# Kernel optimization log

Hardware: AMD Instinct MI355X
Metric: run time of the kernel (lower is better)

## Reference

```python
import jax, jax.numpy as jnp
import numpy as np
from jax import lax

B, L, D, H, N, V, K = 2, 1024, 512, 8, 4, 32000, 64
HD = D // H


def layer_norm(x, g, b, eps=1e-5):
    m = jnp.mean(x, axis=-1, keepdims=True)
    v = jnp.var(x, axis=-1, keepdims=True)
    return (x - m) * lax.rsqrt(v + eps) * g + b


def setup_inputs() -> dict:
    ks = jax.random.split(jax.random.key(0), 16)
    s = 0.02
    return {
        "x_q": jax.random.normal(ks[0], (B, L, D), jnp.float32),
        "x": jax.random.randint(ks[1], (B, L), 0, V, jnp.int32),
        "E_slots": jax.random.normal(ks[2], (V, D), jnp.float32),
        "rhos": jax.random.uniform(ks[3], (N,), jnp.float32, 0.9, 0.999),
        "C_seq": jax.random.uniform(ks[4], (B, L, N), jnp.float32),
        "c_base": jax.random.uniform(ks[5], (B, K, N), jnp.float32),
        "unique_slots": jax.random.randint(ks[6], (B, K), 0, V, jnp.int32),
        "pad_mask": jnp.ones((B, K), jnp.bool_),
        "Wq": jax.random.normal(ks[7], (D, D), jnp.float32) * s,
        "Wk": jax.random.normal(ks[8], (D, D), jnp.float32) * s,
        "Wv": jax.random.normal(ks[9], (D, D), jnp.float32) * s,
        "Wo": jax.random.normal(ks[10], (D, D), jnp.float32) * s,
        "W_pe": jax.random.normal(ks[11], (N, D), jnp.float32) * s,
        "ln_kv_g": jnp.ones((D,), jnp.float32),
        "ln_kv_b": jnp.zeros((D,), jnp.float32),
        "ln_q_g": jnp.ones((D,), jnp.float32),
        "ln_q_b": jnp.zeros((D,), jnp.float32),
    }


def reference(x_q, x, E_slots, rhos, C_seq, c_base, unique_slots, pad_mask,
              Wq, Wk, Wv, Wo, W_pe, ln_kv_g, ln_kv_b, ln_q_g, ln_q_b):
    # --- projections (dropout is eval-mode identity) ---
    memory_base = layer_norm(E_slots, ln_kv_g, ln_kv_b)          # [V,D]
    E_k = (memory_base @ Wk).reshape(V, H, HD)                   # [V,H,hd]
    E_v = (memory_base @ Wv).reshape(V, H, HD)
    P_gate = (C_seq + 1.0) @ W_pe                                # [B,L,D]
    Q = layer_norm(x_q * P_gate, ln_q_g, ln_q_b) @ Wq            # [B,L,D]

    # --- initial EMA state from history ---
    safe = jnp.maximum(unique_slots, 0)                          # [B,K]
    ek0 = E_k[safe]                                              # [B,K,H,hd]
    ev0 = E_v[safe]
    outer0 = ek0[..., :, None] * ev0[..., None, :]               # [B,K,H,hd,hd]
    cb = c_base * pad_mask[..., None].astype(c_base.dtype)
    S0 = jnp.einsum('bkn,bkhij->bhnij', cb, outer0).astype(jnp.float32)  # [B,H,N,hd,hd]

    W_pe_hn = W_pe.reshape(N, H, HD).transpose(1, 0, 2)          # [H,N,hd]
    rhos_b = rhos[None, None, :, None, None]

    Qh = Q.reshape(B, L, H, HD).transpose(1, 0, 2, 3)            # [L,B,H,hd]
    toks = x.T                                                   # [L,B]

    def step(S, inp):
        q_t, tok = inp                                           # [B,H,hd], [B]
        S = S * rhos_b                                           # decay
        q_mod = q_t[:, :, None, :] * W_pe_hn[None]               # [B,H,N,hd]
        o_t = jnp.einsum('bhnd,bhnde->bhe', q_mod, S)            # sum over n, contract d
        ek_t = E_k[tok]                                          # [B,H,hd]
        ev_t = E_v[tok]
        outer = ek_t[..., :, None] * ev_t[..., None, :]          # [B,H,hd,hd]
        S = S + outer[:, :, None]                                # broadcast over N
        return S, o_t

    _, O = lax.scan(step, S0, (Qh, toks))                        # O: [L,B,H,hd]
    O = O.transpose(1, 0, 2, 3).reshape(B, L, D)
    return O @ Wo
```

## Files before the change

kernel.cpp:

```cpp
#include <hip/hip_runtime.h>
#include <stdint.h>

namespace {

constexpr int B = 2, L = 1024, D = 512, H = 8, N = 4, KSL = 64;
constexpr int CHK = 64;
constexpr int NCK = L / CHK;
constexpr int ROWS = B * L + B * KSL;

static_assert(D == 512 && N == 4, "layout assumptions");

typedef _Float16 half8 __attribute__((ext_vector_type(8)));
typedef _Float16 half4v __attribute__((ext_vector_type(4)));
typedef _Float16 half2t __attribute__((ext_vector_type(2)));
typedef float f32x4 __attribute__((ext_vector_type(4)));

__device__ __forceinline__ void gld16(_Float16* lds_dst, const _Float16* gsrc) {
  __builtin_amdgcn_global_load_lds(
      (const __attribute__((address_space(1))) unsigned int*)gsrc,
      (__attribute__((address_space(3))) unsigned int*)lds_dst, 16, 0, 0);
}

__global__ __launch_bounds__(256) void k_pre(
    const float* __restrict__ Wk, const float* __restrict__ Wv,
    const float* __restrict__ Wq, const float* __restrict__ Wo,
    _Float16* __restrict__ WTh,
    const float* __restrict__ E_slots, const int* __restrict__ x,
    const int* __restrict__ uniq, const float* __restrict__ kv_g,
    const float* __restrict__ kv_b, _Float16* __restrict__ lnEh,
    const float* __restrict__ x_q, const float* __restrict__ C_seq,
    const float* __restrict__ W_pe, const float* __restrict__ q_g,
    const float* __restrict__ q_b, _Float16* __restrict__ lnqh) {
  __shared__ _Float16 trh[64 * 66];
  __shared__ float red[8];
  int bid = blockIdx.x;
  int t = threadIdx.x;

  if (bid < 256) {
    int widx = bid >> 6, tile = bid & 63;
    int k0 = (tile >> 3) * 64, n0 = (tile & 7) * 64;
    const float* W = widx == 0 ? Wk : widx == 1 ? Wv : widx == 2 ? Wq : Wo;
#pragma unroll
    for (int i = 0; i < 16; ++i) {
      int idx = t + i * 256, r = idx >> 6, c = idx & 63;
      trh[c * 66 + r] = (_Float16)W[(size_t)(k0 + r) * 512 + n0 + c];
    }
    __syncthreads();
    _Float16* WT = WTh + (size_t)widx * 512 * 512;
#pragma unroll
    for (int i = 0; i < 8; ++i) {
      int idx = t + i * 256, rr = idx >> 5, cc = (idx & 31) * 2;
      half2t v = {trh[rr * 66 + cc], trh[rr * 66 + cc + 1]};
      *(half2t*)&WT[(size_t)(n0 + rr) * 512 + k0 + cc] = v;
    }
    return;
  }

  float vx, vy;
  const float* g;
  const float* bb;
  _Float16* dst;
  int d0 = t * 2;
  if (bid < 256 + ROWS) {
    int r = bid - 256;
    int idx;
    if (r < B * L) {
      idx = x[r];
    } else {
      int u = uniq[r - B * L];
      idx = u > 0 ? u : 0;
    }
    float2 v = *(const float2*)(E_slots + (size_t)idx * D + d0);
    vx = v.x;
    vy = v.y;
    g = kv_g; bb = kv_b;
    dst = lnEh + (size_t)r * D + d0;
  } else {
    int r = bid - 256 - ROWS;
    float c0 = C_seq[r * 4 + 0] + 1.f;
    float c1 = C_seq[r * 4 + 1] + 1.f;
    float c2 = C_seq[r * 4 + 2] + 1.f;
    float c3 = C_seq[r * 4 + 3] + 1.f;
    float p0 = c0 * W_pe[d0] + c1 * W_pe[512 + d0] + c2 * W_pe[1024 + d0] + c3 * W_pe[1536 + d0];
    float p1 = c0 * W_pe[d0 + 1] + c1 * W_pe[513 + d0] + c2 * W_pe[1025 + d0] + c3 * W_pe[1537 + d0];
    float2 xv = *(const float2*)(x_q + (size_t)r * D + d0);
    vx = xv.x * p0;
    vy = xv.y * p1;
    g = q_g; bb = q_b;
    dst = lnqh + (size_t)r * D + d0;
  }
  float s = vx + vy;
  float s2 = vx * vx + vy * vy;
#pragma unroll
  for (int o = 32; o > 0; o >>= 1) {
    s += __shfl_down(s, o);
    s2 += __shfl_down(s2, o);
  }
  if ((t & 63) == 0) {
    red[(t >> 6) * 2] = s;
    red[(t >> 6) * 2 + 1] = s2;
  }
  __syncthreads();
  float S = red[0] + red[2] + red[4] + red[6];
  float S2 = red[1] + red[3] + red[5] + red[7];
  float m = S * (1.f / D);
  float inv = rsqrtf(S2 * (1.f / D) - m * m + 1e-5f);
  half2t o2;
  o2.x = (_Float16)((vx - m) * inv * g[d0] + bb[d0]);
  o2.y = (_Float16)((vy - m) * inv * g[d0 + 1] + bb[d0 + 1]);
  *(half2t*)dst = o2;
}

__global__ __launch_bounds__(256) void k_gemm3(
    const _Float16* __restrict__ A0, const _Float16* __restrict__ Wt0, _Float16* __restrict__ C0, int M0,
    const _Float16* __restrict__ A1, const _Float16* __restrict__ Wt1, _Float16* __restrict__ C1, int M1,
    const _Float16* __restrict__ A2, const _Float16* __restrict__ Wt2, _Float16* __restrict__ C2, int M2) {
  const _Float16* A;
  const _Float16* Wt;
  _Float16* C;
  int M;
  int z = blockIdx.z;
  if (z == 0) { A = A0; Wt = Wt0; C = C0; M = M0; }
  else if (z == 1) { A = A1; Wt = Wt1; C = C1; M = M1; }
  else { A = A2; Wt = Wt2; C = C2; M = M2; }
  int m0 = blockIdx.y * 64;
  if (m0 >= M) return;
  int n0 = blockIdx.x * 64;

  __shared__ _Float16 As[2][64 * 64];
  __shared__ _Float16 Ws[2][64 * 64];
  int t = threadIdx.x;
  int lane = t & 63, w = t >> 6;
  int wr = (w >> 1) * 32, wc = (w & 1) * 32;
  int fr = lane & 15, kg = (lane >> 4) * 8;
  int kq = kg >> 3, fx = fr & 7;
  int pA = kq ^ fx, pB = (4 + kq) ^ fx;

  int srow = t >> 3;
  int sseg = ((t & 7) ^ (srow & 7)) * 8;
  int wbase = w * 512;

  const _Float16* gA = A + (size_t)(m0 + srow) * 512 + sseg;
  const _Float16* gB = Wt + (size_t)(n0 + srow) * 512 + sseg;

  f32x4 zero4 = {0.f, 0.f, 0.f, 0.f};
  f32x4 acc[2][2];
#pragma unroll
  for (int i = 0; i < 2; ++i)
#pragma unroll
    for (int j = 0; j < 2; ++j) acc[i][j] = zero4;

  gld16(&As[0][wbase], gA);
  gld16(&As[0][wbase + 2048], gA + 32 * 512);
  gld16(&Ws[0][wbase], gB);
  gld16(&Ws[0][wbase + 2048], gB + 32 * 512);
  __syncthreads();

  int buf = 0;
  for (int s8 = 0; s8 < 8; ++s8) {
    if (s8 < 7) {
      int k0 = (s8 + 1) * 64;
      gld16(&As[buf ^ 1][wbase], gA + k0);
      gld16(&As[buf ^ 1][wbase + 2048], gA + 32 * 512 + k0);
      gld16(&Ws[buf ^ 1][wbase], gB + k0);
      gld16(&Ws[buf ^ 1][wbase + 2048], gB + 32 * 512 + k0);
    }
    half8 af[2][2], bf[2][2];
#pragma unroll
    for (int mt = 0; mt < 2; ++mt) {
      int row = wr + mt * 16 + fr;
      af[mt][0] = *(const half8*)&As[buf][row * 64 + pA * 8];
      af[mt][1] = *(const half8*)&As[buf][row * 64 + pB * 8];
    }
#pragma unroll
    for (int nt = 0; nt < 2; ++nt) {
      int row = wc + nt * 16 + fr;
      bf[nt][0] = *(const half8*)&Ws[buf][row * 64 + pA * 8];
      bf[nt][1] = *(const half8*)&Ws[buf][row * 64 + pB * 8];
    }
#pragma unroll
    for (int mt = 0; mt < 2; ++mt)
#pragma unroll
      for (int nt = 0; nt < 2; ++nt) {
        acc[mt][nt] = __builtin_amdgcn_mfma_f32_16x16x32_f16(af[mt][0], bf[nt][0], acc[mt][nt], 0, 0, 0);
        acc[mt][nt] = __builtin_amdgcn_mfma_f32_16x16x32_f16(af[mt][1], bf[nt][1], acc[mt][nt], 0, 0, 0);
      }
    if (s8 < 7) __syncthreads();
    buf ^= 1;
  }
  int crow = (lane >> 4) * 4, ccol = lane & 15;
#pragma unroll
  for (int mt = 0; mt < 2; ++mt)
#pragma unroll
    for (int nt = 0; nt < 2; ++nt)
#pragma unroll
      for (int r = 0; r < 4; ++r)
        C[(size_t)(m0 + wr + mt * 16 + crow + r) * 512 + n0 + wc + nt * 16 + ccol] =
            (_Float16)acc[mt][nt][r];
}

__global__ __launch_bounds__(256) void k_gemm64(const _Float16* __restrict__ A,
                                                const _Float16* __restrict__ Wt,
                                                float* __restrict__ C) {
  int m0 = blockIdx.y * 64, n0 = blockIdx.x * 64;
  __shared__ _Float16 As[2][64 * 64];
  __shared__ _Float16 Ws[2][64 * 64];
  int t = threadIdx.x;
  int lane = t & 63, w = t >> 6;
  int wr = (w >> 1) * 32, wc = (w & 1) * 32;
  int fr = lane & 15, kg = (lane >> 4) * 8;
  int kq = kg >> 3, fx = fr & 7;
  int pA = kq ^ fx, pB = (4 + kq) ^ fx;

  int srow = t >> 3;
  int sseg = ((t & 7) ^ (srow & 7)) * 8;
  int wbase = w * 512;

  const _Float16* gA = A + (size_t)(m0 + srow) * 512 + sseg;
  const _Float16* gB = Wt + (size_t)(n0 + srow) * 512 + sseg;

  f32x4 zero4 = {0.f, 0.f, 0.f, 0.f};
  f32x4 acc[2][2];
#pragma unroll
  for (int i = 0; i < 2; ++i)
#pragma unroll
    for (int j = 0; j < 2; ++j) acc[i][j] = zero4;

  gld16(&As[0][wbase], gA);
  gld16(&As[0][wbase + 2048], gA + 32 * 512);
  gld16(&Ws[0][wbase], gB);
  gld16(&Ws[0][wbase + 2048], gB + 32 * 512);
  __syncthreads();

  int buf = 0;
  for (int s8 = 0; s8 < 8; ++s8) {
    if (s8 < 7) {
      int k0 = (s8 + 1) * 64;
      gld16(&As[buf ^ 1][wbase], gA + k0);
      gld16(&As[buf ^ 1][wbase + 2048], gA + 32 * 512 + k0);
      gld16(&Ws[buf ^ 1][wbase], gB + k0);
      gld16(&Ws[buf ^ 1][wbase + 2048], gB + 32 * 512 + k0);
    }
    half8 af[2][2], bf[2][2];
#pragma unroll
    for (int mt = 0; mt < 2; ++mt) {
      int row = wr + mt * 16 + fr;
      af[mt][0] = *(const half8*)&As[buf][row * 64 + pA * 8];
      af[mt][1] = *(const half8*)&As[buf][row * 64 + pB * 8];
    }
#pragma unroll
    for (int nt = 0; nt < 2; ++nt) {
      int row = wc + nt * 16 + fr;
      bf[nt][0] = *(const half8*)&Ws[buf][row * 64 + pA * 8];
      bf[nt][1] = *(const half8*)&Ws[buf][row * 64 + pB * 8];
    }
#pragma unroll
    for (int mt = 0; mt < 2; ++mt)
#pragma unroll
      for (int nt = 0; nt < 2; ++nt) {
        acc[mt][nt] = __builtin_amdgcn_mfma_f32_16x16x32_f16(af[mt][0], bf[nt][0], acc[mt][nt], 0, 0, 0);
        acc[mt][nt] = __builtin_amdgcn_mfma_f32_16x16x32_f16(af[mt][1], bf[nt][1], acc[mt][nt], 0, 0, 0);
      }
    if (s8 < 7) __syncthreads();
    buf ^= 1;
  }
  int crow = (lane >> 4) * 4, ccol = lane & 15;
#pragma unroll
  for (int mt = 0; mt < 2; ++mt)
#pragma unroll
    for (int nt = 0; nt < 2; ++nt)
#pragma unroll
      for (int r = 0; r < 4; ++r)
        C[(size_t)(m0 + wr + mt * 16 + crow + r) * 512 + n0 + wc + nt * 16 + ccol] =
            acc[mt][nt][r];
}

__global__ __launch_bounds__(256) void k_dct(const _Float16* __restrict__ EKh,
                                             const _Float16* __restrict__ EVh,
                                             const float* __restrict__ rhos,
                                             const float* __restrict__ c_base,
                                             _Float16* __restrict__ DCt,
                                             _Float16* __restrict__ S0t) {
  constexpr int LDH = 72;
  __shared__ _Float16 ekt[64 * LDH];
  __shared__ _Float16 evt[64 * LDH];
  __shared__ _Float16 dtab[4][64];
  int bid = blockIdx.x;
  int t = threadIdx.x;
  bool is_s0 = bid >= B * H * NCK;
  int row = t >> 2, seg = (t & 3) * 16;
  size_t grow;
  if (!is_s0) {
    int c = bid % NCK, h = (bid / NCK) % H, b = bid / (NCK * H);
    grow = (size_t)(b * L + c * CHK + row) * 512 + h * 64 + seg;
    int nn = t >> 6, uu = t & 63;
    dtab[nn][uu] = (_Float16)exp2f((float)(CHK - uu) * log2f(rhos[nn]));
  } else {
    int bh = bid - B * H * NCK;
    int h = bh % H, b = bh / H;
    grow = (size_t)(B * L + b * KSL + row) * 512 + h * 64 + seg;
    int nn = t >> 6, uu = t & 63;
    dtab[nn][uu] = (_Float16)c_base[(b * KSL + uu) * N + nn];
  }
  half8 e0 = *(const half8*)(EKh + grow);
  half8 e1 = *(const half8*)(EKh + grow + 8);
  half8 v0 = *(const half8*)(EVh + grow);
  half8 v1 = *(const half8*)(EVh + grow + 8);
#pragma unroll
  for (int i = 0; i < 8; ++i) {
    ekt[(seg + i) * LDH + row] = e0[i];
    ekt[(seg + 8 + i) * LDH + row] = e1[i];
    evt[(seg + i) * LDH + row] = v0[i];
    evt[(seg + 8 + i) * LDH + row] = v1[i];
  }
  __syncthreads();

  int lane = t & 63, w = t >> 6;
  int wr = (w >> 1) * 32, wc = (w & 1) * 32;
  int fr = lane & 15, kg = (lane >> 4) * 8;
  int crow = (lane >> 4) * 4, ccol = lane & 15;

  half8 ef[2][2], bf[2][2];
#pragma unroll
  for (int mt = 0; mt < 2; ++mt)
#pragma unroll
    for (int ks = 0; ks < 2; ++ks)
      ef[mt][ks] = *(const half8*)&evt[(wr + mt * 16 + fr) * LDH + ks * 32 + kg];
#pragma unroll
  for (int nt = 0; nt < 2; ++nt)
#pragma unroll
    for (int ks = 0; ks < 2; ++ks)
      bf[nt][ks] = *(const half8*)&ekt[(wc + nt * 16 + fr) * LDH + ks * 32 + kg];

  f32x4 zero4 = {0.f, 0.f, 0.f, 0.f};
#pragma unroll
  for (int n = 0; n < 4; ++n) {
    half8 dec0 = *(const half8*)&dtab[n][kg];
    half8 dec1 = *(const half8*)&dtab[n][32 + kg];
    half8 af0a = ef[0][0] * dec0, af0b = ef[0][1] * dec1;
    half8 af1a = ef[1][0] * dec0, af1b = ef[1][1] * dec1;
    f32x4 acc[2][2];
#pragma unroll
    for (int i = 0; i < 2; ++i)
#pragma unroll
      for (int j = 0; j < 2; ++j) acc[i][j] = zero4;
#pragma unroll
    for (int nt = 0; nt < 2; ++nt) {
      acc[0][nt] = __builtin_amdgcn_mfma_f32_16x16x32_f16(af0a, bf[nt][0], acc[0][nt], 0, 0, 0);
      acc[0][nt] = __builtin_amdgcn_mfma_f32_16x16x32_f16(af0b, bf[nt][1], acc[0][nt], 0, 0, 0);
      acc[1][nt] = __builtin_amdgcn_mfma_f32_16x16x32_f16(af1a, bf[nt][0], acc[1][nt], 0, 0, 0);
      acc[1][nt] = __builtin_amdgcn_mfma_f32_16x16x32_f16(af1b, bf[nt][1], acc[1][nt], 0, 0, 0);
    }
    _Float16* dp = is_s0 ? S0t + ((size_t)(bid - B * H * NCK) * N + n) * 4096
                         : DCt + ((size_t)bid * N + n) * 4096;
#pragma unroll
    for (int mt = 0; mt < 2; ++mt)
#pragma unroll
      for (int nt = 0; nt < 2; ++nt)
#pragma unroll
        for (int r = 0; r < 4; ++r)
          dp[(wr + mt * 16 + crow + r) * 64 + wc + nt * 16 + ccol] = (_Float16)acc[mt][nt][r];
  }
}

__global__ void k_gscan(const _Float16* __restrict__ S0t, const _Float16* __restrict__ DCt,
                        const float* __restrict__ rhos, _Float16* __restrict__ GT) {
  int bhn = blockIdx.x >> 2, sl = blockIdx.x & 3;
  int n = bhn % N, bh = bhn / N;
  float rho = rhos[n];
  float rhoC = exp2f(64.f * log2f(rho));
  int off = sl * 1024 + threadIdx.x * 4;
  half4v dc[NCK];
#pragma unroll
  for (int c = 0; c < NCK; ++c)
    dc[c] = *(const half4v*)(DCt + ((size_t)(bh * NCK + c) * N + n) * 4096 + off);
  half4v s0 = *(const half4v*)(S0t + (size_t)bhn * 4096 + off);
  float gv[4];
#pragma unroll
  for (int i = 0; i < 4; ++i) gv[i] = rho * (float)s0[i];
  _Float16* gp = GT + (size_t)bhn * NCK * 4096 + off;
#pragma unroll
  for (int cc = 0; cc < NCK; ++cc) {
    half4v o;
#pragma unroll
    for (int i = 0; i < 4; ++i) o[i] = (_Float16)gv[i];
    *(half4v*)(gp + (size_t)cc * 4096) = o;
#pragma unroll
    for (int i = 0; i < 4; ++i) gv[i] = rhoC * gv[i] + (float)dc[cc][i];
  }
}

__global__ __launch_bounds__(256) void k_chunk(
    const _Float16* __restrict__ Qh, const _Float16* __restrict__ EKh,
    const _Float16* __restrict__ EVh, const _Float16* __restrict__ GT,
    const float* __restrict__ W_pe, const float* __restrict__ rhos,
    _Float16* __restrict__ OAh) {
  int bid = blockIdx.x;
  int c = bid % NCK, h = (bid / NCK) % H, b = bid / (NCK * H);
  constexpr int LDH = 72;
  __shared__ _Float16 qs[64 * LDH];
  __shared__ _Float16 eks[64 * LDH];
  __shared__ _Float16 evt[64 * LDH];
  __shared__ _Float16 gts[4][64 * LDH];
  __shared__ _Float16 wsm[64 * LDH];
  __shared__ _Float16 wpeh[4][64];
  __shared__ float rup[4][64];
  __shared__ float rvi[4][64];
  int t = threadIdx.x;
  {
    int row = t >> 2, seg = (t & 3) * 16;
    size_t grow = (size_t)(b * L + c * CHK + row) * 512 + h * 64 + seg;
    half8 q0 = *(const half8*)(Qh + grow);
    half8 q1 = *(const half8*)(Qh + grow + 8);
    half8 k0 = *(const half8*)(EKh + grow);
    half8 k1 = *(const half8*)(EKh + grow + 8);
    half8 v0 = *(const half8*)(EVh + grow);
    half8 v1 = *(const half8*)(EVh + grow + 8);
    *(half8*)&qs[row * LDH + seg] = q0;
    *(half8*)&qs[row * LDH + seg + 8] = q1;
    *(half8*)&eks[row * LDH + seg] = k0;
    *(half8*)&eks[row * LDH + seg + 8] = k1;
#pragma unroll
    for (int i = 0; i < 8; ++i) {
      evt[(seg + i) * LDH + row] = v0[i];
      evt[(seg + 8 + i) * LDH + row] = v1[i];
    }
#pragma unroll
    for (int n = 0; n < 4; ++n) {
      const _Float16* gpp = GT + (((size_t)(b * H + h) * N + n) * NCK + c) * 4096 + row * 64 + seg;
      *(half8*)&gts[n][row * LDH + seg] = *(const half8*)gpp;
      *(half8*)&gts[n][row * LDH + seg + 8] = *(const half8*)(gpp + 8);
    }
    int nn = t >> 6, dd = t & 63;
    float l2r = log2f(rhos[nn]);
    wpeh[nn][dd] = (_Float16)W_pe[nn * 512 + h * 64 + dd];
    rup[nn][dd] = exp2f((float)dd * l2r);
    rvi[nn][dd] = exp2f(-(float)dd * l2r);
  }
  __syncthreads();

  int lane = t & 63, w = t >> 6;
  int u0 = w * 16;
  int fr = lane & 15, kg = (lane >> 4) * 8;
  int crow = (lane >> 4) * 4, ccol = lane & 15;

  half8 qf0 = *(const half8*)&qs[(u0 + fr) * LDH + kg];
  half8 qf1 = *(const half8*)&qs[(u0 + fr) * LDH + 32 + kg];

  f32x4 zero4 = {0.f, 0.f, 0.f, 0.f};
  f32x4 oa[4], wacc[4];
#pragma unroll
  for (int i = 0; i < 4; ++i) { oa[i] = zero4; wacc[i] = zero4; }

#pragma unroll
  for (int n = 0; n < 4; ++n) {
    half8 am0 = qf0 * (*(const half8*)&wpeh[n][kg]);
    half8 am1 = qf1 * (*(const half8*)&wpeh[n][32 + kg]);
    float ru[4];
#pragma unroll
    for (int r = 0; r < 4; ++r) ru[r] = rup[n][u0 + crow + r];
#pragma unroll
    for (int et = 0; et < 4; ++et) {
      f32x4 ta = zero4;
      ta = __builtin_amdgcn_mfma_f32_16x16x32_f16(
          am0, *(const half8*)&gts[n][(et * 16 + fr) * LDH + kg], ta, 0, 0, 0);
      ta = __builtin_amdgcn_mfma_f32_16x16x32_f16(
          am1, *(const half8*)&gts[n][(et * 16 + fr) * LDH + 32 + kg], ta, 0, 0, 0);
#pragma unroll
      for (int r = 0; r < 4; ++r) oa[et][r] += ru[r] * ta[r];
    }
#pragma unroll
    for (int vt = 0; vt < 4; ++vt) {
      f32x4 sa = zero4;
      sa = __builtin_amdgcn_mfma_f32_16x16x32_f16(
          am0, *(const half8*)&eks[(vt * 16 + fr) * LDH + kg], sa, 0, 0, 0);
      sa = __builtin_amdgcn_mfma_f32_16x16x32_f16(
          am1, *(const half8*)&eks[(vt * 16 + fr) * LDH + 32 + kg], sa, 0, 0, 0);
      int v = vt * 16 + ccol;
      float rv = rvi[n][v];
#pragma unroll
      for (int r = 0; r < 4; ++r) {
        int u = u0 + crow + r;
        float coef = (v < u) ? ru[r] * rv : 0.f;
        wacc[vt][r] += coef * sa[r];
      }
    }
  }
#pragma unroll
  for (int vt = 0; vt < 4; ++vt)
#pragma unroll
    for (int r = 0; r < 4; ++r)
      wsm[(u0 + crow + r) * LDH + vt * 16 + ccol] = (_Float16)wacc[vt][r];
  half8 wf0 = *(const half8*)&wsm[(u0 + fr) * LDH + kg];
  half8 wf1 = *(const half8*)&wsm[(u0 + fr) * LDH + 32 + kg];
#pragma unroll
  for (int et = 0; et < 4; ++et) {
    oa[et] = __builtin_amdgcn_mfma_f32_16x16x32_f16(
        wf0, *(const half8*)&evt[(et * 16 + fr) * LDH + kg], oa[et], 0, 0, 0);
    oa[et] = __builtin_amdgcn_mfma_f32_16x16x32_f16(
        wf1, *(const half8*)&evt[(et * 16 + fr) * LDH + 32 + kg], oa[et], 0, 0, 0);
  }
#pragma unroll
  for (int et = 0; et < 4; ++et)
#pragma unroll
    for (int r = 0; r < 4; ++r)
      OAh[(size_t)(b * L + c * CHK + u0 + crow + r) * 512 + h * 64 + et * 16 + ccol] =
          (_Float16)oa[et][r];
}

}

extern "C" void kernel_launch(void* const* d_in, const int* in_sizes, int n_in,
                              void* d_out, int out_size, void* d_ws, size_t ws_size,
                              hipStream_t stream) {
  const float* x_q = (const float*)d_in[0];
  const int* x = (const int*)d_in[1];
  const float* E_slots = (const float*)d_in[2];
  const float* rhos = (const float*)d_in[3];
  const float* C_seq = (const float*)d_in[4];
  const float* c_base = (const float*)d_in[5];
  const int* uniq = (const int*)d_in[6];
  const float* Wq = (const float*)d_in[8];
  const float* Wk = (const float*)d_in[9];
  const float* Wv = (const float*)d_in[10];
  const float* Wo = (const float*)d_in[11];
  const float* W_pe = (const float*)d_in[12];
  const float* ln_kv_g = (const float*)d_in[13];
  const float* ln_kv_b = (const float*)d_in[14];
  const float* ln_q_g = (const float*)d_in[15];
  const float* ln_q_b = (const float*)d_in[16];
  float* out = (float*)d_out;

  _Float16* hb = (_Float16*)d_ws;
  _Float16* lnEh = hb;
  _Float16* lnqh = lnEh + 1114112;
  _Float16* WTh = lnqh + 1048576;
  _Float16* EKh = WTh + 1048576;
  _Float16* EVh = EKh + 1114112;
  _Float16* Qh = EVh + 1114112;
  _Float16* DCt = Qh + 1048576;
  _Float16* S0t = DCt + 4194304;
  _Float16* GT = S0t + 262144;
  _Float16* OAh = GT + 4194304;

  const _Float16* WTk = WTh;
  const _Float16* WTv = WTh + 262144;
  const _Float16* WTq = WTh + 524288;
  const _Float16* WTo = WTh + 786432;

  k_pre<<<256 + ROWS + B * L, 256, 0, stream>>>(
      Wk, Wv, Wq, Wo, WTh, E_slots, x, uniq, ln_kv_g, ln_kv_b, lnEh,
      x_q, C_seq, W_pe, ln_q_g, ln_q_b, lnqh);
  k_gemm3<<<dim3(8, 34, 3), 256, 0, stream>>>(lnEh, WTk, EKh, ROWS,
                                              lnEh, WTv, EVh, ROWS,
                                              lnqh, WTq, Qh, B * L);
  k_dct<<<B * H * NCK + B * H, 256, 0, stream>>>(EKh, EVh, rhos, c_base, DCt, S0t);
  k_gscan<<<B * H * N * 4, 256, 0, stream>>>(S0t, DCt, rhos, GT);
  k_chunk<<<B * H * NCK, 256, 0, stream>>>(Qh, EKh, EVh, GT, W_pe, rhos, OAh);
  k_gemm64<<<dim3(8, 32), 256, 0, stream>>>(OAh, WTo, out);
}
```

Measured before the change: 44.63 us.

## Fuse K/V projection GEMMs with chunk outer-product kernel

Merges the separate K and V projection blocks into one block that shares the A tile and computes both accumulators. The per-chunk decayed outer-product (DCt/S0t) work is then done in the same block from registers through shared memory, which removes the k_dct launch and its reload of EKh/EVh. In exchange each block uses more registers and shared memory, which may reduce occupancy, and the fused blocks carry a longer serial tail.

```diff
diff --git a/kernel.cpp b/kernel.cpp
--- a/kernel.cpp
+++ b/kernel.cpp
@@ -111,92 +111,230 @@
   *(half2t*)dst = o2;
 }
 
-__global__ __launch_bounds__(256) void k_gemm3(
-    const _Float16* __restrict__ A0, const _Float16* __restrict__ Wt0, _Float16* __restrict__ C0, int M0,
-    const _Float16* __restrict__ A1, const _Float16* __restrict__ Wt1, _Float16* __restrict__ C1, int M1,
-    const _Float16* __restrict__ A2, const _Float16* __restrict__ Wt2, _Float16* __restrict__ C2, int M2) {
-  const _Float16* A;
-  const _Float16* Wt;
-  _Float16* C;
-  int M;
+__global__ __launch_bounds__(256) void k_gemmkv(
+    const _Float16* __restrict__ lnEh, const _Float16* __restrict__ lnqh,
+    const _Float16* __restrict__ WTk, const _Float16* __restrict__ WTv,
+    const _Float16* __restrict__ WTq,
+    _Float16* __restrict__ EKh, _Float16* __restrict__ EVh, _Float16* __restrict__ Qh,
+    const float* __restrict__ rhos, const float* __restrict__ c_base,
+    _Float16* __restrict__ DCt, _Float16* __restrict__ S0t) {
+  __shared__ _Float16 smem[24576];
+  _Float16* As = smem;
+  _Float16* B1 = smem + 8192;
+  _Float16* B2 = smem + 16384;
+
   int z = blockIdx.z;
-  if (z == 0) { A = A0; Wt = Wt0; C = C0; M = M0; }
-  else if (z == 1) { A = A1; Wt = Wt1; C = C1; M = M1; }
-  else { A = A2; Wt = Wt2; C = C2; M = M2; }
-  int m0 = blockIdx.y * 64;
-  if (m0 >= M) return;
-  int n0 = blockIdx.x * 64;
-
-  __shared__ _Float16 As[2][64 * 64];
-  __shared__ _Float16 Ws[2][64 * 64];
+  int m0 = blockIdx.y * 64, n0 = blockIdx.x * 64;
   int t = threadIdx.x;
   int lane = t & 63, w = t >> 6;
   int wr = (w >> 1) * 32, wc = (w & 1) * 32;
   int fr = lane & 15, kg = (lane >> 4) * 8;
   int kq = kg >> 3, fx = fr & 7;
   int pA = kq ^ fx, pB = (4 + kq) ^ fx;
-
   int srow = t >> 3;
   int sseg = ((t & 7) ^ (srow & 7)) * 8;
   int wbase = w * 512;
-
-  const _Float16* gA = A + (size_t)(m0 + srow) * 512 + sseg;
-  const _Float16* gB = Wt + (size_t)(n0 + srow) * 512 + sseg;
+  int crow = (lane >> 4) * 4, ccol = lane & 15;
 
   f32x4 zero4 = {0.f, 0.f, 0.f, 0.f};
-  f32x4 acc[2][2];
+
+  if (z == 1) {
+    if (m0 >= B * L) return;
+    const _Float16* gA = lnqh + (size_t)(m0 + srow) * 512 + sseg;
+    const _Float16* gB = WTq + (size_t)(n0 + srow) * 512 + sseg;
+    f32x4 acc[2][2];
+#pragma unroll
+    for (int i = 0; i < 2; ++i)
+#pragma unroll
+      for (int j = 0; j < 2; ++j) acc[i][j] = zero4;
+    gld16(&As[wbase], gA);
+    gld16(&As[wbase + 2048], gA + 32 * 512);
+    gld16(&B1[wbase], gB);
+    gld16(&B1[wbase + 2048], gB + 32 * 512);
+    __syncthreads();
+    int buf = 0;
+    for (int s8 = 0; s8 < 8; ++s8) {
+      if (s8 < 7) {
+        int k0 = (s8 + 1) * 64;
+        gld16(&As[(buf ^ 1) * 4096 + wbase], gA + k0);
+        gld16(&As[(buf ^ 1) * 4096 + wbase + 2048], gA + 32 * 512 + k0);
+        gld16(&B1[(buf ^ 1) * 4096 + wbase], gB + k0);
+        gld16(&B1[(buf ^ 1) * 4096 + wbase + 2048], gB + 32 * 512 + k0);
+      }
+      half8 af[2][2], bf[2][2];
+#pragma unroll
+      for (int mt = 0; mt < 2; ++mt) {
+        int row = wr + mt * 16 + fr;
+        af[mt][0] = *(const half8*)&As[buf * 4096 + row * 64 + pA * 8];
+        af[mt][1] = *(const half8*)&As[buf * 4096 + row * 64 + pB * 8];
+      }
+#pragma unroll
+      for (int nt = 0; nt < 2; ++nt) {
+        int row = wc + nt * 16 + fr;
+        bf[nt][0] = *(const half8*)&B1[buf * 4096 + row * 64 + pA * 8];
+        bf[nt][1] = *(const half8*)&B1[buf * 4096 + row * 64 + pB * 8];
+      }
+#pragma unroll
+      for (int mt = 0; mt < 2; ++mt)
+#pragma unroll
+        for (int nt = 0; nt < 2; ++nt) {
+          acc[mt][nt] = __builtin_amdgcn_mfma_f32_16x16x32_f16(af[mt][0], bf[nt][0], acc[mt][nt], 0, 0, 0);
+          acc[mt][nt] = __builtin_amdgcn_mfma_f32_16x16x32_f16(af[mt][1], bf[nt][1], acc[mt][nt], 0, 0, 0);
+        }
+      if (s8 < 7) __syncthreads();
+      buf ^= 1;
+    }
+#pragma unroll
+    for (int mt = 0; mt < 2; ++mt)
+#pragma unroll
+      for (int nt = 0; nt < 2; ++nt)
+#pragma unroll
+        for (int r = 0; r < 4; ++r)
+          Qh[(size_t)(m0 + wr + mt * 16 + crow + r) * 512 + n0 + wc + nt * 16 + ccol] =
+              (_Float16)acc[mt][nt][r];
+    return;
+  }
+
+  const _Float16* gA = lnEh + (size_t)(m0 + srow) * 512 + sseg;
+  const _Float16* gK = WTk + (size_t)(n0 + srow) * 512 + sseg;
+  const _Float16* gV = WTv + (size_t)(n0 + srow) * 512 + sseg;
+  f32x4 acck[2][2], accv[2][2];
 #pragma unroll
   for (int i = 0; i < 2; ++i)
 #pragma unroll
-    for (int j = 0; j < 2; ++j) acc[i][j] = zero4;
-
-  gld16(&As[0][wbase], gA);
-  gld16(&As[0][wbase + 2048], gA + 32 * 512);
-  gld16(&Ws[0][wbase], gB);
-  gld16(&Ws[0][wbase + 2048], gB + 32 * 512);
+    for (int j = 0; j < 2; ++j) { acck[i][j] = zero4; accv[i][j] = zero4; }
+
+  gld16(&As[wbase], gA);
+  gld16(&As[wbase + 2048], gA + 32 * 512);
+  gld16(&B1[wbase], gK);
+  gld16(&B1[wbase + 2048], gK + 32 * 512);
+  gld16(&B2[wbase], gV);
+  gld16(&B2[wbase + 2048], gV + 32 * 512);
   __syncthreads();
 
   int buf = 0;
   for (int s8 = 0; s8 < 8; ++s8) {
     if (s8 < 7) {
       int k0 = (s8 + 1) * 64;
-      gld16(&As[buf ^ 1][wbase], gA + k0);
-      gld16(&As[buf ^ 1][wbase + 2048], gA + 32 * 512 + k0);
-      gld16(&Ws[buf ^ 1][wbase], gB + k0);
-      gld16(&Ws[buf ^ 1][wbase + 2048], gB + 32 * 512 + k0);
-    }
-    half8 af[2][2], bf[2][2];
+      gld16(&As[(buf ^ 1) * 4096 + wbase], gA + k0);
+      gld16(&As[(buf ^ 1) * 4096 + wbase + 2048], gA + 32 * 512 + k0);
+      gld16(&B1[(buf ^ 1) * 4096 + wbase], gK + k0);
+      gld16(&B1[(buf ^ 1) * 4096 + wbase + 2048], gK + 32 * 512 + k0);
+      gld16(&B2[(buf ^ 1) * 4096 + wbase], gV + k0);
+      gld16(&B2[(buf ^ 1) * 4096 + wbase + 2048], gV + 32 * 512 + k0);
+    }
+    half8 af[2][2], bk[2][2], bv[2][2];
 #pragma unroll
     for (int mt = 0; mt < 2; ++mt) {
       int row = wr + mt * 16 + fr;
-      af[mt][0] = *(const half8*)&As[buf][row * 64 + pA * 8];
-      af[mt][1] = *(const half8*)&As[buf][row * 64 + pB * 8];
+      af[mt][0] = *(const half8*)&As[buf * 4096 + row * 64 + pA * 8];
+      af[mt][1] = *(const half8*)&As[buf * 4096 + row * 64 + pB * 8];
     }
 #pragma unroll
     for (int nt = 0; nt < 2; ++nt) {
       int row = wc + nt * 16 + fr;
-      bf[nt][0] = *(const half8*)&Ws[buf][row * 64 + pA * 8];
-      bf[nt][1] = *(const half8*)&Ws[buf][row * 64 + pB * 8];
+      bk[nt][0] = *(const half8*)&B1[buf * 4096 + row * 64 + pA * 8];
+      bk[nt][1] = *(const half8*)&B1[buf * 4096 + row * 64 + pB * 8];
+      bv[nt][0] = *(const half8*)&B2[buf * 4096 + row * 64 + pA * 8];
+      bv[nt][1] = *(const half8*)&B2[buf * 4096 + row * 64 + pB * 8];
     }
 #pragma unroll
     for (int mt = 0; mt < 2; ++mt)
 #pragma unroll
       for (int nt = 0; nt < 2; ++nt) {
-        acc[mt][nt] = __builtin_amdgcn_mfma_f32_16x16x32_f16(af[mt][0], bf[nt][0], acc[mt][nt], 0, 0, 0);
-        acc[mt][nt] = __builtin_amdgcn_mfma_f32_16x16x32_f16(af[mt][1], bf[nt][1], acc[mt][nt], 0, 0, 0);
+        acck[mt][nt] = __builtin_amdgcn_mfma_f32_16x16x32_f16(af[mt][0], bk[nt][0], acck[mt][nt], 0, 0, 0);
+        acck[mt][nt] = __builtin_amdgcn_mfma_f32_16x16x32_f16(af[mt][1], bk[nt][1], acck[mt][nt], 0, 0, 0);
+        accv[mt][nt] = __builtin_amdgcn_mfma_f32_16x16x32_f16(af[mt][0], bv[nt][0], accv[mt][nt], 0, 0, 0);
+        accv[mt][nt] = __builtin_amdgcn_mfma_f32_16x16x32_f16(af[mt][1], bv[nt][1], accv[mt][nt], 0, 0, 0);
       }
     if (s8 < 7) __syncthreads();
     buf ^= 1;
   }
-  int crow = (lane >> 4) * 4, ccol = lane & 15;
 #pragma unroll
   for (int mt = 0; mt < 2; ++mt)
 #pragma unroll
     for (int nt = 0; nt < 2; ++nt)
 #pragma unroll
-      for (int r = 0; r < 4; ++r)
-        C[(size_t)(m0 + wr + mt * 16 + crow + r) * 512 + n0 + wc + nt * 16 + ccol] =
-            (_Float16)acc[mt][nt][r];
+      for (int r = 0; r < 4; ++r) {
+        size_t gi = (size_t)(m0 + wr + mt * 16 + crow + r) * 512 + n0 + wc + nt * 16 + ccol;
+        EKh[gi] = (_Float16)acck[mt][nt][r];
+        EVh[gi] = (_Float16)accv[mt][nt][r];
+      }
+
+  __syncthreads();
+  constexpr int LDH = 72;
+  _Float16* ekt = smem;
+  _Float16* evt = smem + 4608;
+  _Float16* dtab = smem + 9216;
+  bool is_s0 = m0 >= B * L;
+  int h = n0 >> 6;
+  int bb_, cc_ = 0;
+  if (!is_s0) {
+    bb_ = m0 >> 10;
+    cc_ = (m0 & 1023) >> 6;
+  } else {
+    bb_ = (m0 - B * L) >> 6;
+  }
+  {
+    int nn = t >> 6, uu = t & 63;
+    float dv;
+    if (!is_s0) dv = exp2f((float)(CHK - uu) * log2f(rhos[nn]));
+    else dv = c_base[(bb_ * KSL + uu) * N + nn];
+    dtab[nn * 64 + uu] = (_Float16)dv;
+  }
+#pragma unroll
+  for (int mt = 0; mt < 2; ++mt)
+#pragma unroll
+    for (int nt = 0; nt < 2; ++nt)
+#pragma unroll
+      for (int r = 0; r < 4; ++r) {
+        int u = wr + mt * 16 + crow + r;
+        int dcol = wc + nt * 16 + ccol;
+        ekt[dcol * LDH + u] = (_Float16)acck[mt][nt][r];
+        evt[dcol * LDH + u] = (_Float16)accv[mt][nt][r];
+      }
+  __syncthreads();
+
+  half8 ef[2][2], bfk[2][2];
+#pragma unroll
+  for (int mt = 0; mt < 2; ++mt)
+#pragma unroll
+    for (int ks = 0; ks < 2; ++ks)
+      ef[mt][ks] = *(const half8*)&evt[(wr + mt * 16 + fr) * LDH + ks * 32 + kg];
+#pragma unroll
+  for (int nt = 0; nt < 2; ++nt)
+#pragma unroll
+    for (int ks = 0; ks < 2; ++ks)
+      bfk[nt][ks] = *(const half8*)&ekt[(wc + nt * 16 + fr) * LDH + ks * 32 + kg];
+
+#pragma unroll
+  for (int n = 0; n < 4; ++n) {
+    half8 dec0 = *(const half8*)&dtab[n * 64 + kg];
+    half8 dec1 = *(const half8*)&dtab[n * 64 + 32 + kg];
+    half8 af0a = ef[0][0] * dec0, af0b = ef[0][1] * dec1;
+    half8 af1a = ef[1][0] * dec0, af1b = ef[1][1] * dec1;
+    f32x4 acc[2][2];
+#pragma unroll
+    for (int i = 0; i < 2; ++i)
+#pragma unroll
+      for (int j = 0; j < 2; ++j) acc[i][j] = zero4;
+#pragma unroll
+    for (int nt = 0; nt < 2; ++nt) {
+      acc[0][nt] = __builtin_amdgcn_mfma_f32_16x16x32_f16(af0a, bfk[nt][0], acc[0][nt], 0, 0, 0);
+      acc[0][nt] = __builtin_amdgcn_mfma_f32_16x16x32_f16(af0b, bfk[nt][1], acc[0][nt], 0, 0, 0);
+      acc[1][nt] = __builtin_amdgcn_mfma_f32_16x16x32_f16(af1a, bfk[nt][0], acc[1][nt], 0, 0, 0);
+      acc[1][nt] = __builtin_amdgcn_mfma_f32_16x16x32_f16(af1b, bfk[nt][1], acc[1][nt], 0, 0, 0);
+    }
+    _Float16* dp = is_s0 ? S0t + (((size_t)bb_ * H + h) * N + n) * 4096
+                         : DCt + (((((size_t)bb_ * H + h) * NCK) + cc_) * N + n) * 4096;
+#pragma unroll
+    for (int mt = 0; mt < 2; ++mt)
+#pragma unroll
+      for (int nt = 0; nt < 2; ++nt)
+#pragma unroll
+        for (int r = 0; r < 4; ++r)
+          dp[(wr + mt * 16 + crow + r) * 64 + wc + nt * 16 + ccol] = (_Float16)acc[mt][nt][r];
+  }
 }
 
 __global__ __launch_bounds__(256) void k_gemm64(const _Float16* __restrict__ A,
@@ -273,94 +411,6 @@
       for (int r = 0; r < 4; ++r)
         C[(size_t)(m0 + wr + mt * 16 + crow + r) * 512 + n0 + wc + nt * 16 + ccol] =
             acc[mt][nt][r];
-}
-
-__global__ __launch_bounds__(256) void k_dct(const _Float16* __restrict__ EKh,
-                                             const _Float16* __restrict__ EVh,
-                                             const float* __restrict__ rhos,
-                                             const float* __restrict__ c_base,
-                                             _Float16* __restrict__ DCt,
-                                             _Float16* __restrict__ S0t) {
-  constexpr int LDH = 72;
-  __shared__ _Float16 ekt[64 * LDH];
-  __shared__ _Float16 evt[64 * LDH];
-  __shared__ _Float16 dtab[4][64];
-  int bid = blockIdx.x;
-  int t = threadIdx.x;
-  bool is_s0 = bid >= B * H * NCK;
-  int row = t >> 2, seg = (t & 3) * 16;
-  size_t grow;
-  if (!is_s0) {
-    int c = bid % NCK, h = (bid / NCK) % H, b = bid / (NCK * H);
-    grow = (size_t)(b * L + c * CHK + row) * 512 + h * 64 + seg;
-    int nn = t >> 6, uu = t & 63;
-    dtab[nn][uu] = (_Float16)exp2f((float)(CHK - uu) * log2f(rhos[nn]));
-  } else {
-    int bh = bid - B * H * NCK;
-    int h = bh % H, b = bh / H;
-    grow = (size_t)(B * L + b * KSL + row) * 512 + h * 64 + seg;
-    int nn = t >> 6, uu = t & 63;
-    dtab[nn][uu] = (_Float16)c_base[(b * KSL + uu) * N + nn];
-  }
-  half8 e0 = *(const half8*)(EKh + grow);
-  half8 e1 = *(const half8*)(EKh + grow + 8);
-  half8 v0 = *(const half8*)(EVh + grow);
-  half8 v1 = *(const half8*)(EVh + grow + 8);
-#pragma unroll
-  for (int i = 0; i < 8; ++i) {
-    ekt[(seg + i) * LDH + row] = e0[i];
-    ekt[(seg + 8 + i) * LDH + row] = e1[i];
-    evt[(seg + i) * LDH + row] = v0[i];
-    evt[(seg + 8 + i) * LDH + row] = v1[i];
-  }
-  __syncthreads();
-
-  int lane = t & 63, w = t >> 6;
-  int wr = (w >> 1) * 32, wc = (w & 1) * 32;
-  int fr = lane & 15, kg = (lane >> 4) * 8;
-  int crow = (lane >> 4) * 4, ccol = lane & 15;
-
-  half8 ef[2][2], bf[2][2];
-#pragma unroll
-  for (int mt = 0; mt < 2; ++mt)
-#pragma unroll
-    for (int ks = 0; ks < 2; ++ks)
-      ef[mt][ks] = *(const half8*)&evt[(wr + mt * 16 + fr) * LDH + ks * 32 + kg];
-#pragma unroll
-  for (int nt = 0; nt < 2; ++nt)
-#pragma unroll
-    for (int ks = 0; ks < 2; ++ks)
-      bf[nt][ks] = *(const half8*)&ekt[(wc + nt * 16 + fr) * LDH + ks * 32 + kg];
-
-  f32x4 zero4 = {0.f, 0.f, 0.f, 0.f};
-#pragma unroll
-  for (int n = 0; n < 4; ++n) {
-    half8 dec0 = *(const half8*)&dtab[n][kg];
-    half8 dec1 = *(const half8*)&dtab[n][32 + kg];
-    half8 af0a = ef[0][0] * dec0, af0b = ef[0][1] * dec1;
-    half8 af1a = ef[1][0] * dec0, af1b = ef[1][1] * dec1;
-    f32x4 acc[2][2];
-#pragma unroll
-    for (int i = 0; i < 2; ++i)
-#pragma unroll
-      for (int j = 0; j < 2; ++j) acc[i][j] = zero4;
-#pragma unroll
-    for (int nt = 0; nt < 2; ++nt) {
-      acc[0][nt] = __builtin_amdgcn_mfma_f32_16x16x32_f16(af0a, bf[nt][0], acc[0][nt], 0, 0, 0);
-      acc[0][nt] = __builtin_amdgcn_mfma_f32_16x16x32_f16(af0b, bf[nt][1], acc[0][nt], 0, 0, 0);
-      acc[1][nt] = __builtin_amdgcn_mfma_f32_16x16x32_f16(af1a, bf[nt][0], acc[1][nt], 0, 0, 0);
-      acc[1][nt] = __builtin_amdgcn_mfma_f32_16x16x32_f16(af1b, bf[nt][1], acc[1][nt], 0, 0, 0);
-    }
-    _Float16* dp = is_s0 ? S0t + ((size_t)(bid - B * H * NCK) * N + n) * 4096
-                         : DCt + ((size_t)bid * N + n) * 4096;
-#pragma unroll
-    for (int mt = 0; mt < 2; ++mt)
-#pragma unroll
-      for (int nt = 0; nt < 2; ++nt)
-#pragma unroll
-        for (int r = 0; r < 4; ++r)
-          dp[(wr + mt * 16 + crow + r) * 64 + wc + nt * 16 + ccol] = (_Float16)acc[mt][nt][r];
-  }
 }
 
 __global__ void k_gscan(const _Float16* __restrict__ S0t, const _Float16* __restrict__ DCt,
@@ -551,10 +601,8 @@
   k_pre<<<256 + ROWS + B * L, 256, 0, stream>>>(
       Wk, Wv, Wq, Wo, WTh, E_slots, x, uniq, ln_kv_g, ln_kv_b, lnEh,
       x_q, C_seq, W_pe, ln_q_g, ln_q_b, lnqh);
-  k_gemm3<<<dim3(8, 34, 3), 256, 0, stream>>>(lnEh, WTk, EKh, ROWS,
-                                              lnEh, WTv, EVh, ROWS,
-                                              lnqh, WTq, Qh, B * L);
-  k_dct<<<B * H * NCK + B * H, 256, 0, stream>>>(EKh, EVh, rhos, c_base, DCt, S0t);
+  k_gemmkv<<<dim3(8, 34, 2), 256, 0, stream>>>(lnEh, lnqh, WTk, WTv, WTq,
+                                               EKh, EVh, Qh, rhos, c_base, DCt, S0t);
   k_gscan<<<B * H * N * 4, 256, 0, stream>>>(S0t, DCt, rhos, GT);
   k_chunk<<<B * H * NCK, 256, 0, stream>>>(Qh, EKh, EVh, GT, W_pe, rhos, OAh);
   k_gemm64<<<dim3(8, 32), 256, 0, stream>>>(OAh, WTo, out);
```

New measurement: 43.31 us, median of 2. -2.9%, faster.
